# Performance work log

Hardware: AMD Instinct MI355X
Metric: run time of the kernel (lower is better)

Reference implementation:

```python
import jax, jax.numpy as jnp
import numpy as np

T_START = 0.0
T_END = 1.0
STEPS = 10
HID = 1024
BATCH = 8192


def setup_inputs() -> dict:
    key = jax.random.key(0)
    ks = jax.random.split(key, 7)
    s1 = 1.0 / np.sqrt(HID + 1)
    s2 = 1.0 / np.sqrt(HID)
    return {
        "h": jax.random.normal(ks[0], (BATCH, HID), dtype=jnp.float32),
        "W1": jax.random.uniform(ks[1], (HID + 1, HID), jnp.float32, -s1, s1),
        "b1": jax.random.uniform(ks[2], (HID,), jnp.float32, -s1, s1),
        "W2": jax.random.uniform(ks[3], (HID, HID), jnp.float32, -s2, s2),
        "b2": jax.random.uniform(ks[4], (HID,), jnp.float32, -s2, s2),
        "W3": jax.random.uniform(ks[5], (HID, HID), jnp.float32, -s2, s2),
        "b3": jax.random.uniform(ks[6], (HID,), jnp.float32, -s2, s2),
    }


def reference(h, W1, b1, W2, b2, W3, b3):
    dt = (T_END - T_START) / STEPS

    def dynamics(t, h):
        # concat(h, t*ones) @ W1 == h @ W1[:-1] + t * W1[-1]; keep explicit concat for clarity
        t_vec = jnp.full((h.shape[0], 1), t, dtype=h.dtype)
        x = jnp.concatenate([h, t_vec], axis=1)
        x = jnp.tanh(x @ W1 + b1)
        x = jnp.tanh(x @ W2 + b2)
        return x @ W3 + b3

    def rk4_step(h, t):
        k1 = dynamics(t, h)
        k2 = dynamics(t + dt / 2, h + dt / 2 * k1)
        k3 = dynamics(t + dt / 2, h + dt / 2 * k2)
        k4 = dynamics(t + dt, h + dt * k3)
        return h + dt / 6 * (k1 + 2 * k2 + 2 * k3 + k4), None

    ts = T_START + dt * jnp.arange(STEPS, dtype=h.dtype)
    h_final, _ = jax.lax.scan(rk4_step, h, ts)
    return h_final
```

## Files before the change

kernel.cpp:

```cpp
#include <hip/hip_runtime.h>


typedef __attribute__((ext_vector_type(8))) __bf16 bf16x8;
typedef __attribute__((ext_vector_type(4))) float f32x4;
typedef __attribute__((ext_vector_type(8))) float f32x8;
typedef __attribute__((ext_vector_type(16))) float f32x16;
typedef __attribute__((ext_vector_type(8))) unsigned short us8;
typedef __attribute__((ext_vector_type(4))) int i32x4;
typedef __attribute__((ext_vector_type(8))) int i32x8;
typedef unsigned short ushort_t;
typedef unsigned char u8;

#define SCALE_ONE  0x7F7F7F7Fu
#define SCALE_INV32 0x7A7A7A7Au

#define GLOAD16(gp, lp) \
  __builtin_amdgcn_global_load_lds((const __attribute__((address_space(1))) unsigned int*)(gp), \
                                   (__attribute__((address_space(3))) unsigned int*)(lp), 16, 0, 0)

__device__ __forceinline__ ushort_t f2bf(float f) {
  union { float f; unsigned u; } v; v.f = f;
  unsigned r = v.u + 0x7fffu + ((v.u >> 16) & 1u);
  return (ushort_t)(r >> 16);
}
__device__ __forceinline__ float b2f(ushort_t u) {
  union { unsigned u; float f; } v; v.u = ((unsigned)u) << 16; return v.f;
}
__device__ __forceinline__ float fast_tanh(float x) {
  float e = __expf(2.0f * x);
  return 1.0f - 2.0f * __builtin_amdgcn_rcpf(e + 1.0f);
}
__device__ __forceinline__ uint2 pack_fp8x8(const float* v) {
  int a = __builtin_amdgcn_cvt_pk_fp8_f32(v[0], v[1], 0, false);
  a = __builtin_amdgcn_cvt_pk_fp8_f32(v[2], v[3], a, true);
  int b = __builtin_amdgcn_cvt_pk_fp8_f32(v[4], v[5], 0, false);
  b = __builtin_amdgcn_cvt_pk_fp8_f32(v[6], v[7], b, true);
  return make_uint2((unsigned)a, (unsigned)b);
}
__device__ __forceinline__ void fp8x4_to_f32(unsigned q, float* o) {
  o[0] = __builtin_amdgcn_cvt_f32_fp8(q, 0);
  o[1] = __builtin_amdgcn_cvt_f32_fp8(q, 1);
  o[2] = __builtin_amdgcn_cvt_f32_fp8(q, 2);
  o[3] = __builtin_amdgcn_cvt_f32_fp8(q, 3);
}
__device__ __forceinline__ void fp8x8_to_f32(uint2 q, float* o) {
  fp8x4_to_f32(q.x, o); fp8x4_to_f32(q.y, o + 4);
}

__global__ void transpose_bf16(const float* __restrict__ in, ushort_t* __restrict__ out) {
  __shared__ float tile[32][33];
  const int bx = blockIdx.x * 32, by = blockIdx.y * 32;
  const int tx = threadIdx.x, ty = threadIdx.y;
#pragma unroll
  for (int i = 0; i < 32; i += 8)
    tile[ty + i][tx] = in[(size_t)(by + ty + i) * 1024 + bx + tx];
  __syncthreads();
#pragma unroll
  for (int i = 0; i < 32; i += 8)
    out[(size_t)(bx + ty + i) * 1024 + by + tx] = f2bf(tile[tx][ty + i]);
}

__global__ void transpose_fp8(const float* __restrict__ in, u8* __restrict__ out) {
  __shared__ float tile[32][33];
  const int bx = blockIdx.x * 32, by = blockIdx.y * 32;
  const int tx = threadIdx.x, ty = threadIdx.y;
#pragma unroll
  for (int i = 0; i < 32; i += 8)
    tile[ty + i][tx] = in[(size_t)(by + ty + i) * 1024 + bx + tx];
  __syncthreads();
#pragma unroll
  for (int i = 0; i < 32; i += 8) {
    const float v = 32.f * tile[tx][ty + i];
    int r = __builtin_amdgcn_cvt_pk_fp8_f32(v, v, 0, false);
    out[(size_t)(bx + ty + i) * 1024 + by + tx] = (u8)(r & 0xFF);
  }
}

__global__ void conv_bf16(const float* __restrict__ in, ushort_t* __restrict__ out) {
  size_t i = ((size_t)blockIdx.x * 256 + threadIdx.x) * 4;
  float4 v = *(const float4*)&in[i];
  ushort4 o;
  o.x = f2bf(v.x); o.y = f2bf(v.y); o.z = f2bf(v.z); o.w = f2bf(v.w);
  *(ushort4*)&out[i] = o;
}

__global__ void c31_kernel(const ushort_t* __restrict__ W1t, const float* __restrict__ b3,
                           float* __restrict__ c31) {
  const int j = blockIdx.x * 256 + threadIdx.x;
  float acc = 0.f;
  for (int c = 0; c < 128; ++c) {
    const us8 w = *(const us8*)&W1t[(size_t)j * 1024 + c * 8];
    const f32x8 b = *(const f32x8*)&b3[c * 8];
#pragma unroll
    for (int e = 0; e < 8; ++e) acc += b2f(w[e]) * b[e];
  }
  c31[j] = acc;
}

__global__ void xtfold(const u8* __restrict__ a, const u8* __restrict__ b,
                       const u8* __restrict__ c, const u8* __restrict__ d,
                       ushort_t* __restrict__ XT) {
  const size_t i = ((size_t)blockIdx.x * 256 + threadIdx.x) * 8;
  float va[8], vb[8], vc[8], vd[8];
  fp8x8_to_f32(*(const uint2*)&a[i], va);
  fp8x8_to_f32(*(const uint2*)&b[i], vb);
  fp8x8_to_f32(*(const uint2*)&c[i], vc);
  fp8x8_to_f32(*(const uint2*)&d[i], vd);
  const us8 xo = *(const us8*)&XT[i];
  us8 xn;
#pragma unroll
  for (int e = 0; e < 8; ++e)
    xn[e] = f2bf(b2f(xo[e]) + va[e] + 2.f * (vb[e] + vc[e]) + vd[e]);
  *(us8*)&XT[i] = xn;
}

template<int MODE>
__global__ void __launch_bounds__(256, 2)
gemm_bf16(const ushort_t* __restrict__ Ag, const ushort_t* __restrict__ Bg,
          const float* __restrict__ bias,
          ushort_t* __restrict__ outb, u8* __restrict__ out8,
          const float* __restrict__ h0f, float* __restrict__ outf)
{
  constexpr int K = 1024, NCOL = 1024, NT = 16;
  constexpr float DT = 0.1f;
  __shared__ __align__(16) ushort_t lds[2][16384];

  const int bid = blockIdx.x;
  const int nb = (int)gridDim.x >> 3;
  const int logical = (bid & 7) * nb + (bid >> 3);
  const int bm0 = (logical >> 3) * 128;
  const int bn0 = (logical & 7) * 128;

  const int tid = threadIdx.x;
  const int w = tid >> 6, l = tid & 63;
  const int wr = w >> 1, wc = w & 1;

  const int srow = l >> 3;
  const int sclog = (l & 7) ^ srow;
  const size_t gA0 = (size_t)(bm0 + w * 32 + srow) * K + sclog * 8;
  const size_t gB0 = (size_t)(bn0 + w * 32 + srow) * K + sclog * 8;
  const int ldsAo = w * 2048 + l * 8;
  const int ldsBo = 8192 + w * 2048 + l * 8;

#define STAGEB(s, t1) do { \
    const ushort_t* ga = Ag + gA0 + (size_t)(t1) * 64; \
    const ushort_t* gb = Bg + gB0 + (size_t)(t1) * 64; \
    GLOAD16(ga,          &lds[s][ldsAo]); \
    GLOAD16(ga + 8 * K,  &lds[s][ldsAo + 512]); \
    GLOAD16(ga + 16 * K, &lds[s][ldsAo + 1024]); \
    GLOAD16(ga + 24 * K, &lds[s][ldsAo + 1536]); \
    GLOAD16(gb,          &lds[s][ldsBo]); \
    GLOAD16(gb + 8 * K,  &lds[s][ldsBo + 512]); \
    GLOAD16(gb + 16 * K, &lds[s][ldsBo + 1024]); \
    GLOAD16(gb + 24 * K, &lds[s][ldsBo + 1536]); } while (0)

  const int r = l & 15, kb = l >> 4, xr = r & 7;
  const int aRow = (wr * 64 + r) * 64;
  const int bRow = 8192 + (wc * 64 + r) * 64;
  const int c0 = ((0 | kb) ^ xr) * 8;
  const int c1 = ((4 | kb) ^ xr) * 8;

  f32x4 acc[4][4];
#pragma unroll
  for (int m = 0; m < 4; ++m)
#pragma unroll
    for (int n = 0; n < 4; ++n) acc[m][n] = (f32x4){0.f, 0.f, 0.f, 0.f};

  STAGEB(0, 0);

  for (int t = 0; t < NT; ++t) {
    const int cur = t & 1;
    __builtin_amdgcn_s_barrier();
    if (t + 1 < NT) {
      STAGEB(cur ^ 1, t + 1);
      asm volatile("s_waitcnt vmcnt(8)" ::: "memory");
    } else {
      asm volatile("s_waitcnt vmcnt(0)" ::: "memory");
    }
    __builtin_amdgcn_s_barrier();
    __builtin_amdgcn_sched_barrier(0);

    const ushort_t* Lb = &lds[cur][0];
    bf16x8 av[4], bv[4];
#pragma unroll
    for (int m = 0; m < 4; ++m) av[m] = *(const bf16x8*)(Lb + aRow + m * 1024 + c0);
#pragma unroll
    for (int n = 0; n < 4; ++n) bv[n] = *(const bf16x8*)(Lb + bRow + n * 1024 + c0);
    __builtin_amdgcn_s_setprio(1);
#pragma unroll
    for (int m = 0; m < 4; ++m)
#pragma unroll
      for (int n = 0; n < 4; ++n)
        acc[m][n] = __builtin_amdgcn_mfma_f32_16x16x32_bf16(av[m], bv[n], acc[m][n], 0, 0, 0);
    __builtin_amdgcn_s_setprio(0);
#pragma unroll
    for (int m = 0; m < 4; ++m) av[m] = *(const bf16x8*)(Lb + aRow + m * 1024 + c1);
#pragma unroll
    for (int n = 0; n < 4; ++n) bv[n] = *(const bf16x8*)(Lb + bRow + n * 1024 + c1);
    __builtin_amdgcn_s_setprio(1);
#pragma unroll
    for (int m = 0; m < 4; ++m)
#pragma unroll
      for (int n = 0; n < 4; ++n)
        acc[m][n] = __builtin_amdgcn_mfma_f32_16x16x32_bf16(av[m], bv[n], acc[m][n], 0, 0, 0);
    __builtin_amdgcn_s_setprio(0);
  }
#undef STAGEB

  __syncthreads();
  ushort_t* C = &lds[0][0];
  const int er = (l >> 4) * 4;
  const int ec = l & 15;
#pragma unroll
  for (int n = 0; n < 4; ++n) {
    const int lc = wc * 64 + n * 16 + ec;
#pragma unroll
    for (int m = 0; m < 4; ++m) {
#pragma unroll
      for (int j = 0; j < 4; ++j) {
        const int lr = wr * 64 + m * 16 + er + j;
        C[lr * 136 + lc] = f2bf(acc[m][n][j]);
      }
    }
  }
  __syncthreads();

  constexpr float DT6 = DT / 6.f;
#pragma unroll
  for (int i = 0; i < 8; ++i) {
    const int chunk = tid + i * 256;
    const int row = chunk >> 4;
    const int cc = chunk & 15;
    const int col0 = bn0 + cc * 8;
    const us8 kv8 = *(const us8*)&C[row * 136 + cc * 8];
    const size_t gidx = (size_t)(bm0 + row) * NCOL + col0;

    if (MODE == 0) {
      float v[8];
#pragma unroll
      for (int e = 0; e < 8; ++e) v[e] = 32.f * b2f(kv8[e]);
      *(uint2*)&out8[gidx] = pack_fp8x8(v);
    } else if (MODE == 1) {
      const f32x8 b = *(const f32x8*)&bias[col0];
      float v[8];
#pragma unroll
      for (int e = 0; e < 8; ++e) v[e] = fast_tanh(b2f(kv8[e]) + b[e]);
      *(us8*)&outb[gidx] = kv8;
      *(uint2*)&out8[gidx] = pack_fp8x8(v);
    } else {
      const f32x8 b = *(const f32x8*)&bias[col0];
      const f32x8 h8 = *(const f32x8*)&h0f[gidx];
      f32x8 o;
#pragma unroll
      for (int e = 0; e < 8; ++e) o[e] = h8[e] + DT6 * b2f(kv8[e]) + b[e];
      *(f32x8*)&outf[gidx] = o;
    }
  }
}

template<int MODE>
__global__ void __launch_bounds__(256, 2)
gemm_fp8(const u8* __restrict__ Ag, const u8* __restrict__ Bg,
         const float* __restrict__ bias, const float* __restrict__ wl,
         const float* __restrict__ c31,
         const ushort_t* __restrict__ hW1r, const ushort_t* __restrict__ GSr,
         const u8* __restrict__ x2a, const u8* __restrict__ x2b, const u8* __restrict__ x2c,
         u8* __restrict__ out8, ushort_t* __restrict__ bfio, ushort_t* __restrict__ hW1w,
         float p0, float p1, float p2, int flag)
{
  constexpr int NT = 16;
  constexpr float DT = 0.1f, DT6 = DT / 6.f;
  __shared__ __align__(16) u8 bufs[2][16384];
  __shared__ __align__(16) ushort_t Cst[128 * 136];

  const int bid = blockIdx.x;
  const int nb = (int)gridDim.x >> 3;
  const int logical = (bid & 7) * nb + (bid >> 3);
  const int bm0 = (logical >> 3) * 128;
  const int bn0 = (logical & 7) * 128;

  const int tid = threadIdx.x;
  const int w = tid >> 6, l = tid & 63;
  const int wr = w >> 1, wc = w & 1;
  const int l31 = l & 31, kg = l >> 5;

  auto srcoff = [](int slot) -> int {
    int rp = slot >> 3, p = slot & 7, q = p ^ (rp & 7);
    return (2 * rp + (q >> 2)) * 1024 + (q & 3) * 16;
  };
  const int so0 = srcoff(tid), so1 = srcoff(256 + tid);
  const u8* gA = Ag + (size_t)bm0 * 1024;
  const u8* gB = Bg + (size_t)bn0 * 1024;
  const int ld0 = tid * 16, ld1 = 4096 + tid * 16;

#define STAGEF(s, t1) do { \
    GLOAD16(gA + so0 + (t1) * 64, &bufs[s][ld0]); \
    GLOAD16(gA + so1 + (t1) * 64, &bufs[s][ld1]); \
    GLOAD16(gB + so0 + (t1) * 64, &bufs[s][8192 + ld0]); \
    GLOAD16(gB + so1 + (t1) * 64, &bufs[s][8192 + ld1]); } while (0)

  auto ldsAddr = [](int r2, int kc) -> int {
    int q = ((r2 & 1) << 2) | kc; int p = q ^ ((r2 >> 1) & 7);
    return (r2 >> 1) * 128 + p * 16;
  };
  const int kc2 = kg * 2;
  const int ra0 = wr * 64 + l31, ra1 = ra0 + 32;
  const int rb0 = wc * 64 + l31, rb1 = rb0 + 32;
  const int aA00 = ldsAddr(ra0, kc2), aA01 = ldsAddr(ra0, kc2 + 1);
  const int aA10 = ldsAddr(ra1, kc2), aA11 = ldsAddr(ra1, kc2 + 1);
  const int bA00 = 8192 + ldsAddr(rb0, kc2), bA01 = 8192 + ldsAddr(rb0, kc2 + 1);
  const int bA10 = 8192 + ldsAddr(rb1, kc2), bA11 = 8192 + ldsAddr(rb1, kc2 + 1);

  f32x16 acc00, acc01, acc10, acc11;
#pragma unroll
  for (int i = 0; i < 16; ++i) { acc00[i] = 0.f; acc01[i] = 0.f; acc10[i] = 0.f; acc11[i] = 0.f; }

#define LD8(dst, o0, o1) do { \
    i32x4 lo_ = *(const i32x4*)(Lb + (o0)); \
    i32x4 hi_ = *(const i32x4*)(Lb + (o1)); \
    dst = (i32x8){lo_[0], lo_[1], lo_[2], lo_[3], hi_[0], hi_[1], hi_[2], hi_[3]}; } while (0)

  STAGEF(0, 0);

  for (int t = 0; t < NT; ++t) {
    const int cur = t & 1;
    __builtin_amdgcn_s_barrier();
    if (t + 1 < NT) {
      STAGEF(cur ^ 1, t + 1);
      asm volatile("s_waitcnt vmcnt(4)" ::: "memory");
    } else {
      asm volatile("s_waitcnt vmcnt(0)" ::: "memory");
    }
    __builtin_amdgcn_s_barrier();
    __builtin_amdgcn_sched_barrier(0);

    const u8* Lb = &bufs[cur][0];
    i32x8 a0, a1, b0, b1;
    LD8(a0, aA00, aA01);
    LD8(a1, aA10, aA11);
    LD8(b0, bA00, bA01);
    LD8(b1, bA10, bA11);
    __builtin_amdgcn_s_setprio(1);
    acc00 = __builtin_amdgcn_mfma_scale_f32_32x32x64_f8f6f4(a0, b0, acc00, 0, 0, 0, SCALE_ONE, 0, SCALE_INV32);
    acc01 = __builtin_amdgcn_mfma_scale_f32_32x32x64_f8f6f4(a0, b1, acc01, 0, 0, 0, SCALE_ONE, 0, SCALE_INV32);
    acc10 = __builtin_amdgcn_mfma_scale_f32_32x32x64_f8f6f4(a1, b0, acc10, 0, 0, 0, SCALE_ONE, 0, SCALE_INV32);
    acc11 = __builtin_amdgcn_mfma_scale_f32_32x32x64_f8f6f4(a1, b1, acc11, 0, 0, 0, SCALE_ONE, 0, SCALE_INV32);
    __builtin_amdgcn_s_setprio(0);
  }
#undef STAGEF

  us8 hw_pre[8], gs_pre[8];
  if (MODE == 3 || MODE == 4) {
#pragma unroll
    for (int i = 0; i < 8; ++i) {
      const int chunk = tid + i * 256;
      const size_t gidx = (size_t)(bm0 + (chunk >> 4)) * 1024 + bn0 + (chunk & 15) * 8;
      hw_pre[i] = *(const us8*)&hW1r[gidx];
    }
  }
  if (MODE == 3 && !flag) {
#pragma unroll
    for (int i = 0; i < 8; ++i) {
      const int chunk = tid + i * 256;
      const size_t gidx = (size_t)(bm0 + (chunk >> 4)) * 1024 + bn0 + (chunk & 15) * 8;
      gs_pre[i] = *(const us8*)&bfio[gidx];
    }
  }
  if (MODE == 4) {
#pragma unroll
    for (int i = 0; i < 8; ++i) {
      const int chunk = tid + i * 256;
      const size_t gidx = (size_t)(bm0 + (chunk >> 4)) * 1024 + bn0 + (chunk & 15) * 8;
      gs_pre[i] = *(const us8*)&GSr[gidx];
    }
  }

#define STORE_ACC(A_, mm, nn) do { \
    _Pragma("unroll") \
    for (int reg = 0; reg < 16; ++reg) { \
      const int lrow = wr * 64 + (mm) * 32 + (reg & 3) + 8 * (reg >> 2) + 4 * kg; \
      const int lcol = wc * 64 + (nn) * 32 + l31; \
      Cst[lrow * 136 + lcol] = f2bf(A_[reg]); } } while (0)
  STORE_ACC(acc00, 0, 0);
  STORE_ACC(acc01, 0, 1);
  STORE_ACC(acc10, 1, 0);
  STORE_ACC(acc11, 1, 1);
#undef STORE_ACC
  __syncthreads();

#pragma unroll
  for (int i = 0; i < 8; ++i) {
    const int chunk = tid + i * 256;
    const int row = chunk >> 4;
    const int cc = chunk & 15;
    const int col0 = bn0 + cc * 8;
    const us8 kv8 = *(const us8*)&Cst[row * 136 + cc * 8];
    const size_t gidx = (size_t)(bm0 + row) * 1024 + col0;

    if (MODE == 2) {
      const f32x8 b = *(const f32x8*)&bias[col0];
      float x2v[8];
#pragma unroll
      for (int e = 0; e < 8; ++e) x2v[e] = fast_tanh(b2f(kv8[e]) + b[e]);
      *(uint2*)&out8[gidx] = pack_fp8x8(x2v);
    } else if (MODE == 3) {
      const f32x8 b  = *(const f32x8*)&bias[col0];
      const f32x8 wv = *(const f32x8*)&wl[col0];
      const f32x8 cv = *(const f32x8*)&c31[col0];
      const us8 hw = hw_pre[i];
      float x1v[8]; us8 gs;
      if (flag) {
#pragma unroll
        for (int e = 0; e < 8; ++e) {
          const float g = b2f(kv8[e]);
          gs[e] = f2bf(g);
          x1v[e] = fast_tanh(b2f(hw[e]) + p1 * (g + cv[e]) + b[e] + p2 * wv[e]);
        }
      } else {
        const us8 og = gs_pre[i];
#pragma unroll
        for (int e = 0; e < 8; ++e) {
          const float g = b2f(kv8[e]);
          gs[e] = f2bf(b2f(og[e]) + p0 * g);
          x1v[e] = fast_tanh(b2f(hw[e]) + p1 * (g + cv[e]) + b[e] + p2 * wv[e]);
        }
      }
      *(us8*)&bfio[gidx] = gs;
      *(uint2*)&out8[gidx] = pack_fp8x8(x1v);
    } else {
      const f32x8 b  = *(const f32x8*)&bias[col0];
      const f32x8 wv = *(const f32x8*)&wl[col0];
      const f32x8 cv = *(const f32x8*)&c31[col0];
      const us8 hw = hw_pre[i];
      const us8 gs = gs_pre[i];
      float va[8], vb[8], vc[8], vd[8];
      fp8x8_to_f32(*(const uint2*)&x2a[gidx], va);
      fp8x8_to_f32(*(const uint2*)&x2b[gidx], vb);
      fp8x8_to_f32(*(const uint2*)&x2c[gidx], vc);
      fp8x8_to_f32(*(const uint2*)&Ag[gidx], vd);
      us8 xtn;
      if (flag) {
#pragma unroll
        for (int e = 0; e < 8; ++e)
          xtn[e] = f2bf(va[e] + 2.f * (vb[e] + vc[e]) + vd[e]);
      } else {
        const us8 xo = *(const us8*)&bfio[gidx];
#pragma unroll
        for (int e = 0; e < 8; ++e)
          xtn[e] = f2bf(b2f(xo[e]) + va[e] + 2.f * (vb[e] + vc[e]) + vd[e]);
      }
      *(us8*)&bfio[gidx] = xtn;
      float x1v[8]; us8 o1;
#pragma unroll
      for (int e = 0; e < 8; ++e) {
        const float hn = b2f(hw[e]) + DT6 * (b2f(gs[e]) + b2f(kv8[e])) + DT * cv[e];
        o1[e] = f2bf(hn);
        x1v[e] = fast_tanh(hn + b[e] + p2 * wv[e]);
      }
      *(us8*)&hW1w[gidx] = o1;
      *(uint2*)&out8[gidx] = pack_fp8x8(x1v);
    }
  }
}

extern "C" void kernel_launch(void* const* d_in, const int* in_sizes, int n_in,
                              void* d_out, int out_size, void* d_ws, size_t ws_size,
                              hipStream_t stream) {
  (void)in_sizes; (void)n_in; (void)out_size; (void)ws_size;
  const float* h_in = (const float*)d_in[0];
  const float* W1   = (const float*)d_in[1];
  const float* b1   = (const float*)d_in[2];
  const float* W2   = (const float*)d_in[3];
  const float* b2   = (const float*)d_in[4];
  const float* W3   = (const float*)d_in[5];
  const float* b3   = (const float*)d_in[6];
  const float* W1last = W1 + (size_t)1024 * 1024;

  char* ws = (char*)d_ws;
  ushort_t* W1t   = (ushort_t*)(ws);
  u8*       W2t8  = (u8*)      (ws + (2ull << 20));
  u8*       Bt318 = (u8*)      (ws + (3ull << 20));
  float*    c31   = (float*)   (ws + (4ull << 20));
  ushort_t* hW1b  = (ushort_t*)(ws + (8ull << 20));
  u8*       x1    = (u8*)      (ws + (24ull << 20));
  u8*       x2s0  = (u8*)      (ws + (32ull << 20));
  u8*       x2s1  = (u8*)      (ws + (40ull << 20));
  u8*       x2s2  = (u8*)      (ws + (48ull << 20));
  u8*       x2s3  = (u8*)      (ws + (56ull << 20));
  ushort_t* XT    = (ushort_t*)(ws + (64ull << 20));
  ushort_t* GS    = (ushort_t*)d_out;
  ushort_t* hb    = (ushort_t*)d_out;
  float*    OUT   = (float*)d_out;

  const float dt = 0.1f;
  constexpr int GRID = 512, BLK = 256;
  dim3 tb(32, 8), tg(32, 32);

  transpose_bf16<<<tg, tb, 0, stream>>>(W1, W1t);
  transpose_fp8 <<<tg, tb, 0, stream>>>(W2, W2t8);
  conv_bf16<<<1024, 256, 0, stream>>>(W3, XT);
  conv_bf16<<<8192, 256, 0, stream>>>(h_in, hb);
  c31_kernel<<<4, 256, 0, stream>>>(W1t, b3, c31);
  gemm_bf16<0><<<64, BLK, 0, stream>>>(W1t, XT, nullptr, nullptr, Bt318, nullptr, nullptr);
  gemm_bf16<1><<<GRID, BLK, 0, stream>>>(hb, W1t, b1, hW1b, x1, nullptr, nullptr);

  for (int step = 0; step < 10; ++step) {
    const float t0 = step * dt;
    gemm_fp8<2><<<GRID, BLK, 0, stream>>>(x1, W2t8, b2, nullptr, nullptr, nullptr, nullptr,
                                          nullptr, nullptr, nullptr, x2s0, nullptr, nullptr,
                                          0.f, 0.f, 0.f, 0);
    gemm_fp8<3><<<GRID, BLK, 0, stream>>>(x2s0, Bt318, b1, W1last, c31, hW1b, nullptr,
                                          nullptr, nullptr, nullptr, x1, GS, nullptr,
                                          1.f, 0.5f * dt, t0 + 0.5f * dt, 1);
    gemm_fp8<2><<<GRID, BLK, 0, stream>>>(x1, W2t8, b2, nullptr, nullptr, nullptr, nullptr,
                                          nullptr, nullptr, nullptr, x2s1, nullptr, nullptr,
                                          0.f, 0.f, 0.f, 0);
    gemm_fp8<3><<<GRID, BLK, 0, stream>>>(x2s1, Bt318, b1, W1last, c31, hW1b, nullptr,
                                          nullptr, nullptr, nullptr, x1, GS, nullptr,
                                          2.f, 0.5f * dt, t0 + 0.5f * dt, 0);
    gemm_fp8<2><<<GRID, BLK, 0, stream>>>(x1, W2t8, b2, nullptr, nullptr, nullptr, nullptr,
                                          nullptr, nullptr, nullptr, x2s2, nullptr, nullptr,
                                          0.f, 0.f, 0.f, 0);
    gemm_fp8<3><<<GRID, BLK, 0, stream>>>(x2s2, Bt318, b1, W1last, c31, hW1b, nullptr,
                                          nullptr, nullptr, nullptr, x1, GS, nullptr,
                                          2.f, dt, t0 + dt, 0);
    gemm_fp8<2><<<GRID, BLK, 0, stream>>>(x1, W2t8, b2, nullptr, nullptr, nullptr, nullptr,
                                          nullptr, nullptr, nullptr, x2s3, nullptr, nullptr,
                                          0.f, 0.f, 0.f, 0);
    if (step < 9) {
      gemm_fp8<4><<<GRID, BLK, 0, stream>>>(x2s3, Bt318, b1, W1last, c31, hW1b, GS,
                                            x2s0, x2s1, x2s2, x1, XT, hW1b,
                                            0.f, 0.f, t0 + dt, (step == 0));
    }
  }
  xtfold<<<4096, 256, 0, stream>>>(x2s0, x2s1, x2s2, x2s3, XT);

  transpose_bf16<<<tg, tb, 0, stream>>>(W3, W1t);
  gemm_bf16<5><<<GRID, BLK, 0, stream>>>(XT, W1t, b3, nullptr, nullptr, h_in, OUT);
}
```

Before: 1.586 ms.

## Double K-tile depth to 128 per stage and alias epilogue buffer onto staging LDS

The FP8 GEMM main loop now stages 128-wide K slices per iteration instead of 64, halving the number of iterations and barriers. Each iteration issues eight async global-to-LDS loads and two MFMA rounds, with a new row-XOR swizzle layout. The separate epilogue staging buffer is removed and aliased onto the double buffer after a sync, which keeps LDS usage roughly constant. This is meant to cut barrier and loop overhead per MFMA. The cost is more outstanding loads per thread and a changed swizzle that could produce bank conflicts.

Result: faster. 1.492 ms (-5.9%).

```diff
diff --git a/kernel.cpp b/kernel.cpp
--- a/kernel.cpp
+++ b/kernel.cpp
@@ -268,10 +268,9 @@
          u8* __restrict__ out8, ushort_t* __restrict__ bfio, ushort_t* __restrict__ hW1w,
          float p0, float p1, float p2, int flag)
 {
-  constexpr int NT = 16;
+  constexpr int NT = 8;
   constexpr float DT = 0.1f, DT6 = DT / 6.f;
-  __shared__ __align__(16) u8 bufs[2][16384];
-  __shared__ __align__(16) ushort_t Cst[128 * 136];
+  __shared__ __align__(16) u8 bufs[2][32768];
 
   const int bid = blockIdx.x;
   const int nb = (int)gridDim.x >> 3;
@@ -284,32 +283,41 @@
   const int wr = w >> 1, wc = w & 1;
   const int l31 = l & 31, kg = l >> 5;
 
-  auto srcoff = [](int slot) -> int {
-    int rp = slot >> 3, p = slot & 7, q = p ^ (rp & 7);
-    return (2 * rp + (q >> 2)) * 1024 + (q & 3) * 16;
-  };
-  const int so0 = srcoff(tid), so1 = srcoff(256 + tid);
+  int so[4], ldo[4];
+#pragma unroll
+  for (int i = 0; i < 4; ++i) {
+    const int slot = tid + i * 256;
+    const int row = slot >> 3, phys = slot & 7;
+    so[i] = row * 1024 + ((phys ^ (row & 7)) << 4);
+    ldo[i] = slot << 4;
+  }
   const u8* gA = Ag + (size_t)bm0 * 1024;
   const u8* gB = Bg + (size_t)bn0 * 1024;
-  const int ld0 = tid * 16, ld1 = 4096 + tid * 16;
 
 #define STAGEF(s, t1) do { \
-    GLOAD16(gA + so0 + (t1) * 64, &bufs[s][ld0]); \
-    GLOAD16(gA + so1 + (t1) * 64, &bufs[s][ld1]); \
-    GLOAD16(gB + so0 + (t1) * 64, &bufs[s][8192 + ld0]); \
-    GLOAD16(gB + so1 + (t1) * 64, &bufs[s][8192 + ld1]); } while (0)
-
-  auto ldsAddr = [](int r2, int kc) -> int {
-    int q = ((r2 & 1) << 2) | kc; int p = q ^ ((r2 >> 1) & 7);
-    return (r2 >> 1) * 128 + p * 16;
+    GLOAD16(gA + so[0] + (t1) * 128, &bufs[s][ldo[0]]); \
+    GLOAD16(gA + so[1] + (t1) * 128, &bufs[s][ldo[1]]); \
+    GLOAD16(gA + so[2] + (t1) * 128, &bufs[s][ldo[2]]); \
+    GLOAD16(gA + so[3] + (t1) * 128, &bufs[s][ldo[3]]); \
+    GLOAD16(gB + so[0] + (t1) * 128, &bufs[s][16384 + ldo[0]]); \
+    GLOAD16(gB + so[1] + (t1) * 128, &bufs[s][16384 + ldo[1]]); \
+    GLOAD16(gB + so[2] + (t1) * 128, &bufs[s][16384 + ldo[2]]); \
+    GLOAD16(gB + so[3] + (t1) * 128, &bufs[s][16384 + ldo[3]]); } while (0)
+
+  auto ldsAddr = [](int row, int c) -> int {
+    return row * 128 + ((c ^ (row & 7)) << 4);
   };
-  const int kc2 = kg * 2;
   const int ra0 = wr * 64 + l31, ra1 = ra0 + 32;
   const int rb0 = wc * 64 + l31, rb1 = rb0 + 32;
-  const int aA00 = ldsAddr(ra0, kc2), aA01 = ldsAddr(ra0, kc2 + 1);
-  const int aA10 = ldsAddr(ra1, kc2), aA11 = ldsAddr(ra1, kc2 + 1);
-  const int bA00 = 8192 + ldsAddr(rb0, kc2), bA01 = 8192 + ldsAddr(rb0, kc2 + 1);
-  const int bA10 = 8192 + ldsAddr(rb1, kc2), bA11 = 8192 + ldsAddr(rb1, kc2 + 1);
+  const int ck0 = kg * 2, ck1 = 4 + kg * 2;
+  const int a00 = ldsAddr(ra0, ck0), a00b = ldsAddr(ra0, ck0 + 1);
+  const int a10 = ldsAddr(ra1, ck0), a10b = ldsAddr(ra1, ck0 + 1);
+  const int b00 = 16384 + ldsAddr(rb0, ck0), b00b = 16384 + ldsAddr(rb0, ck0 + 1);
+  const int b10 = 16384 + ldsAddr(rb1, ck0), b10b = 16384 + ldsAddr(rb1, ck0 + 1);
+  const int a01 = ldsAddr(ra0, ck1), a01b = ldsAddr(ra0, ck1 + 1);
+  const int a11 = ldsAddr(ra1, ck1), a11b = ldsAddr(ra1, ck1 + 1);
+  const int b01 = 16384 + ldsAddr(rb0, ck1), b01b = 16384 + ldsAddr(rb0, ck1 + 1);
+  const int b11 = 16384 + ldsAddr(rb1, ck1), b11b = 16384 + ldsAddr(rb1, ck1 + 1);
 
   f32x16 acc00, acc01, acc10, acc11;
 #pragma unroll
@@ -327,7 +335,7 @@
     __builtin_amdgcn_s_barrier();
     if (t + 1 < NT) {
       STAGEF(cur ^ 1, t + 1);
-      asm volatile("s_waitcnt vmcnt(4)" ::: "memory");
+      asm volatile("s_waitcnt vmcnt(8)" ::: "memory");
     } else {
       asm volatile("s_waitcnt vmcnt(0)" ::: "memory");
     }
@@ -336,16 +344,26 @@
 
     const u8* Lb = &bufs[cur][0];
     i32x8 a0, a1, b0, b1;
-    LD8(a0, aA00, aA01);
-    LD8(a1, aA10, aA11);
-    LD8(b0, bA00, bA01);
-    LD8(b1, bA10, bA11);
+    LD8(a0, a00, a00b);
+    LD8(a1, a10, a10b);
+    LD8(b0, b00, b00b);
+    LD8(b1, b10, b10b);
     __builtin_amdgcn_s_setprio(1);
     acc00 = __builtin_amdgcn_mfma_scale_f32_32x32x64_f8f6f4(a0, b0, acc00, 0, 0, 0, SCALE_ONE, 0, SCALE_INV32);
     acc01 = __builtin_amdgcn_mfma_scale_f32_32x32x64_f8f6f4(a0, b1, acc01, 0, 0, 0, SCALE_ONE, 0, SCALE_INV32);
     acc10 = __builtin_amdgcn_mfma_scale_f32_32x32x64_f8f6f4(a1, b0, acc10, 0, 0, 0, SCALE_ONE, 0, SCALE_INV32);
     acc11 = __builtin_amdgcn_mfma_scale_f32_32x32x64_f8f6f4(a1, b1, acc11, 0, 0, 0, SCALE_ONE, 0, SCALE_INV32);
     __builtin_amdgcn_s_setprio(0);
+    LD8(a0, a01, a01b);
+    LD8(a1, a11, a11b);
+    LD8(b0, b01, b01b);
+    LD8(b1, b11, b11b);
+    __builtin_amdgcn_s_setprio(1);
+    acc00 = __builtin_amdgcn_mfma_scale_f32_32x32x64_f8f6f4(a0, b0, acc00, 0, 0, 0, SCALE_ONE, 0, SCALE_INV32);
+    acc01 = __builtin_amdgcn_mfma_scale_f32_32x32x64_f8f6f4(a0, b1, acc01, 0, 0, 0, SCALE_ONE, 0, SCALE_INV32);
+    acc10 = __builtin_amdgcn_mfma_scale_f32_32x32x64_f8f6f4(a1, b0, acc10, 0, 0, 0, SCALE_ONE, 0, SCALE_INV32);
+    acc11 = __builtin_amdgcn_mfma_scale_f32_32x32x64_f8f6f4(a1, b1, acc11, 0, 0, 0, SCALE_ONE, 0, SCALE_INV32);
+    __builtin_amdgcn_s_setprio(0);
   }
 #undef STAGEF
 
@@ -375,6 +393,8 @@
     }
   }
 
+  __syncthreads();
+  ushort_t* Cst = (ushort_t*)&bufs[0][0];
 #define STORE_ACC(A_, mm, nn) do { \
     _Pragma("unroll") \
     for (int reg = 0; reg < 16; ++reg) { \
```
